# Kernel optimization log

Measured on AMD Instinct MI355X. Metric: run time of the kernel, lower is better.

## Reference

```python
import jax, jax.numpy as jnp
import numpy as np
from jax import lax

DILATIONS = [1, 2, 4, 8, 16, 32, 64, 128, 256, 512] * 2  # 20 layers
C = 128   # residual channels
K = 2     # kernel size


def _causal_dilated_conv(x, w, b, d):
    # x: [B, C, T], w: [2C, C, K], left-pad by d*(K-1) for causality
    pad = d * (K - 1)
    y = lax.conv_general_dilated(
        x, w, window_strides=(1,), padding=[(pad, 0)],
        rhs_dilation=(d,), dimension_numbers=('NCH', 'OIH', 'NCH'))
    return y + b[None, :, None]


def setup_inputs() -> dict:
    key = jax.random.key(0)
    ks = jax.random.split(key, 5)
    L = len(DILATIONS)
    x = jax.random.normal(ks[0], (4, C, 8192), jnp.float32)
    # 0.05 scale keeps activations stable through 20 residual layers
    w_conv = jax.random.normal(ks[1], (L, 2 * C, C, K), jnp.float32) * 0.05
    b_conv = jax.random.normal(ks[2], (L, 2 * C), jnp.float32) * 0.05
    w_out = jax.random.normal(ks[3], (L, C, C), jnp.float32) * 0.05
    b_out = jax.random.normal(ks[4], (L, C), jnp.float32) * 0.05
    return {"x": x, "w_conv": w_conv, "b_conv": b_conv,
            "w_out": w_out, "b_out": b_out}


def reference(x, w_conv, b_conv, w_out, b_out):
    """WaveNet convolution stack: per layer, causal dilated conv -> gated
    tanh*sigmoid -> 1x1 output conv; residual add; collect skips.
    Returns (output [B,C,T], skips [L,B,C,T])."""
    skips = []
    for i, d in enumerate(DILATIONS):
        h = x
        z = _causal_dilated_conv(x, w_conv[i], b_conv[i], d)  # [B, 2C, T]
        g = jnp.tanh(z[:, :C]) * jax.nn.sigmoid(z[:, C:])      # gated, [B, C, T]
        s = jnp.einsum('oc,bct->bot', w_out[i], g) + b_out[i][None, :, None]
        x = s + h  # residual connection
        skips.append(s)
    return x, jnp.stack(skips)
```

## Files before the change

### kernel.cpp

```cpp
#include <hip/hip_runtime.h>
#include <hip/hip_bf16.h>
#include <stdint.h>

using f32x4  = __attribute__((ext_vector_type(4))) float;
using bf16x8 = __attribute__((ext_vector_type(8))) short;
using bf16x4 = __attribute__((ext_vector_type(4))) short;

#define NB   4
#define NC   128
#define NT   8192
#define TL   64
#define NLAYER 20
#define GROWB 272
#define CONVN (NLAYER * 256 * 256)
#define WOUTN (NLAYER * 128 * 128)

__device__ __forceinline__ short f2b(float f) {
  union { float f; unsigned u; } v; v.f = f;
  unsigned r = v.u + 0x7FFFu + ((v.u >> 16) & 1u);
  return (short)(r >> 16);
}

__device__ __forceinline__ float b2f(short s) {
  union { unsigned u; float f; } v;
  v.u = ((unsigned)(unsigned short)s) << 16;
  return v.f;
}

__device__ __forceinline__ f32x4 mfma16(bf16x8 a, bf16x8 b, f32x4 c) {
  return __builtin_amdgcn_mfma_f32_16x16x32_bf16(a, b, c, 0, 0, 0);
}

__device__ __forceinline__ void gl_lds16(const void* g, void* l) {
  __builtin_amdgcn_global_load_lds(
      (const __attribute__((address_space(1))) void*)g,
      (__attribute__((address_space(3))) void*)l, 16, 0, 0);
}

__global__ void transpose_in(const float* __restrict__ x, short* __restrict__ xtb) {
  __shared__ float tile[64][65];
  const int t0 = blockIdx.x * 64;
  const int c0 = blockIdx.y * 64;
  const int b  = blockIdx.z;
  const int lane = threadIdx.x & 63;
  const int r4   = threadIdx.x >> 6;
  #pragma unroll
  for (int i = 0; i < 16; ++i) {
    const int cl = i * 4 + r4;
    tile[cl][lane] = x[((size_t)(b * NC + c0 + cl)) * NT + t0 + lane];
  }
  __syncthreads();
  #pragma unroll
  for (int i = 0; i < 16; ++i) {
    const int tr = i * 4 + r4;
    const float v = tile[lane][tr];
    const int t = t0 + tr, c = c0 + lane;
    const size_t rowB = ((size_t)(b * NT + t)) * 256;
    const int ci = (c >> 3) ^ (t & 7);
    *(short*)((char*)xtb + rowB + ci * 16 + (c & 7) * 2) = f2b(v);
  }
}

__global__ void pack_weights(const float* __restrict__ w_conv,
                             const float* __restrict__ w_out,
                             short* __restrict__ wcb, short* __restrict__ wob) {
  const int idx = blockIdx.x * 256 + threadIdx.x;
  if (idx < CONVN) {
    const int k = idx & 255, o = (idx >> 8) & 255, lyr = idx >> 16;
    const int tap = k >> 7, c = k & 127;
    wcb[idx] = f2b(w_conv[(((size_t)lyr * 256 + o) * 128 + c) * 2 + tap]);
  } else if (idx < CONVN + WOUTN) {
    const int j = idx - CONVN;
    wob[j] = f2b(w_out[j]);
  }
}

__global__ __launch_bounds__(512, 4)
void wavenet_layer(const short* __restrict__ wcb,
                   const float* __restrict__ b_conv,
                   const short* __restrict__ wob,
                   const float* __restrict__ b_out,
                   const short* __restrict__ xbin,
                   short* __restrict__ xbout,
                   float* __restrict__ out,
                   int layer, int dil, int last)
{
  __shared__ char ldsXP[TL * 256];
  __shared__ char ldsXC[TL * 256];
  __shared__ char ldsG[TL * GROWB];

  const int tid = threadIdx.x;
  const int w   = tid >> 6;
  const int l   = tid & 63;
  const int lh  = l & 15;
  const int lq  = l >> 4;
  const int o0  = 16 * w + lq * 4;
  const int uid = (blockIdx.x & 7) * 64 + (blockIdx.x >> 3);
  const int b   = uid >> 7;
  const int t0  = (uid & 127) * 64;

  {
    const char* xcg = (const char*)xbin + ((size_t)(b * NT + t0)) * 256;
    const int off = w * 2048 + l * 16;
    gl_lds16(xcg + off, ldsXC + off);
    gl_lds16(xcg + off + 1024, ldsXC + off + 1024);
  }
  if (t0 >= dil) {
    const char* xpg = (const char*)xbin + ((size_t)(b * NT + t0 - dil)) * 256;
    const int off = w * 2048 + l * 16;
    gl_lds16(xpg + off, ldsXP + off);
    gl_lds16(xpg + off + 1024, ldsXP + off + 1024);
  } else {
    const int row = tid >> 3, j8 = tid & 7;
    const int tp = t0 + row - dil;
    char* dst = ldsXP + row * 256;
    if (tp >= 0) {
      const char* src = (const char*)xbin + ((size_t)(b * NT + tp)) * 256;
      *(bf16x8*)(dst + j8 * 16)       = *(const bf16x8*)(src + j8 * 16);
      *(bf16x8*)(dst + j8 * 16 + 128) = *(const bf16x8*)(src + j8 * 16 + 128);
    } else {
      bf16x8 z = {0, 0, 0, 0, 0, 0, 0, 0};
      *(bf16x8*)(dst + j8 * 16)       = z;
      *(bf16x8*)(dst + j8 * 16 + 128) = z;
    }
  }
  __syncthreads();

  const f32x4 fz = {0.f, 0.f, 0.f, 0.f};
  f32x4 acc1[2][4];
  #pragma unroll
  for (int mi = 0; mi < 2; ++mi)
    #pragma unroll
    for (int n = 0; n < 4; ++n) acc1[mi][n] = fz;

  const short* wl = wcb + (size_t)layer * 65536;
  #pragma unroll
  for (int ks = 0; ks < 8; ++ks) {
    const bf16x8 a0 = *(const bf16x8*)(wl + (16 * w + lh) * 256 + ks * 32 + lq * 8);
    const bf16x8 a1 = *(const bf16x8*)(wl + (128 + 16 * w + lh) * 256 + ks * 32 + lq * 8);
    const char* base = (ks < 4) ? ldsXP : ldsXC;
    const int dd = (ks < 4) ? dil : 0;
    #pragma unroll
    for (int n = 0; n < 4; ++n) {
      const int tt = n * 16 + lh;
      const int ci = ((ks & 3) * 4 + lq) ^ ((tt - dd) & 7);
      const bf16x8 bb = *(const bf16x8*)(base + tt * 256 + ci * 16);
      acc1[0][n] = mfma16(a0, bb, acc1[0][n]);
      acc1[1][n] = mfma16(a1, bb, acc1[1][n]);
    }
  }

  {
    float ba[4], bs[4];
    #pragma unroll
    for (int r = 0; r < 4; ++r) {
      ba[r] = b_conv[layer * 256 + o0 + r];
      bs[r] = b_conv[layer * 256 + 128 + o0 + r];
    }
    #pragma unroll
    for (int n = 0; n < 4; ++n) {
      bf16x4 g4;
      #pragma unroll
      for (int r = 0; r < 4; ++r) {
        const float za = acc1[0][n][r] + ba[r];
        const float zb = acc1[1][n][r] + bs[r];
        const float th = 1.f - 2.f / (1.f + __expf(2.f * za));
        const float sg = 1.f / (1.f + __expf(-zb));
        g4[r] = f2b(th * sg);
      }
      const int tt = n * 16 + lh;
      *(bf16x4*)(ldsG + tt * GROWB + o0 * 2) = g4;
    }
  }
  __syncthreads();

  f32x4 acc2[4];
  #pragma unroll
  for (int n = 0; n < 4; ++n) acc2[n] = fz;
  const short* wol = wob + (size_t)layer * 16384;
  #pragma unroll
  for (int ks = 0; ks < 4; ++ks) {
    const bf16x8 a = *(const bf16x8*)(wol + (16 * w + lh) * 128 + ks * 32 + lq * 8);
    #pragma unroll
    for (int n = 0; n < 4; ++n) {
      const int tt = n * 16 + lh;
      const bf16x8 bb = *(const bf16x8*)(ldsG + tt * GROWB + ks * 64 + lq * 16);
      acc2[n] = mfma16(a, bb, acc2[n]);
    }
  }

  {
    const size_t XOFFS = (size_t)NB * NC * NT;
    float bo[4];
    #pragma unroll
    for (int r = 0; r < 4; ++r) bo[r] = b_out[layer * 128 + o0 + r];
    #pragma unroll
    for (int n = 0; n < 4; ++n) {
      const int tt = n * 16 + lh;
      const int tg = t0 + tt;
      f32x4 s4;
      #pragma unroll
      for (int r = 0; r < 4; ++r) s4[r] = acc2[n][r] + bo[r];
      #pragma unroll
      for (int r = 0; r < 4; ++r)
        out[XOFFS + ((size_t)((layer * NB + b) * NC + o0 + r)) * NT + tg] = s4[r];
      const int ci = (o0 >> 3) ^ (tt & 7);
      const bf16x4 h4 = *(const bf16x4*)(ldsXC + tt * 256 + ci * 16 + (o0 & 7) * 2);
      f32x4 xn;
      #pragma unroll
      for (int r = 0; r < 4; ++r) xn[r] = s4[r] + b2f(h4[r]);
      if (!last) {
        bf16x4 x4;
        #pragma unroll
        for (int r = 0; r < 4; ++r) x4[r] = f2b(xn[r]);
        *(bf16x4*)((char*)xbout + ((size_t)(b * NT + tg)) * 256 + ci * 16 + (o0 & 7) * 2) = x4;
      } else {
        #pragma unroll
        for (int r = 0; r < 4; ++r)
          out[((size_t)(b * NC + o0 + r)) * NT + tg] = xn[r];
      }
    }
  }
}

extern "C" void kernel_launch(void* const* d_in, const int* in_sizes, int n_in,
                              void* d_out, int out_size, void* d_ws, size_t ws_size,
                              hipStream_t stream) {
  const float* x      = (const float*)d_in[0];
  const float* w_conv = (const float*)d_in[1];
  const float* b_conv = (const float*)d_in[2];
  const float* w_out  = (const float*)d_in[3];
  const float* b_out  = (const float*)d_in[4];
  float* out = (float*)d_out;

  const size_t XTN = (size_t)NB * NT * NC;
  short* xb_a = (short*)d_ws;
  short* xb_b = xb_a + XTN;
  short* wcb  = xb_b + XTN;
  short* wob  = wcb + CONVN;

  pack_weights<<<(CONVN + WOUTN + 255) / 256, 256, 0, stream>>>(w_conv, w_out, wcb, wob);
  transpose_in<<<dim3(NT / 64, NC / 64, NB), 256, 0, stream>>>(x, xb_a);

  static const int dil[NLAYER] = {1, 2, 4, 8, 16, 32, 64, 128, 256, 512,
                                  1, 2, 4, 8, 16, 32, 64, 128, 256, 512};
  for (int i = 0; i < NLAYER; ++i) {
    const short* xbi = (i & 1) ? xb_b : xb_a;
    short*       xbo = (i & 1) ? xb_a : xb_b;
    wavenet_layer<<<dim3(512), 512, 0, stream>>>(
        wcb, b_conv, wob, b_out, xbi, xbo, out, i, dil[i],
        (i == NLAYER - 1) ? 1 : 0);
  }
}
```

Before: 381.6 us.

## Fuse first six dilation layers per block with halo recompute in LDS

Adds a kernel that runs layers with dilation 1..32 back-to-back inside one block. It loads a 64-step halo plus the 64-step tile into LDS and recomputes the halo region, so the activation stays in LDS between layers. This replaces 12 of the 20 per-layer launches and cuts their global round trips of the activation, at the cost of about double the MFMA work for the halo, larger LDS use (64KB) and possibly lower occupancy. The input transpose is also vectorised to write 16-byte bf16 chunks instead of single shorts.

```diff
diff --git a/kernel.cpp b/kernel.cpp
--- a/kernel.cpp
+++ b/kernel.cpp
@@ -51,13 +51,16 @@
   }
   __syncthreads();
   #pragma unroll
-  for (int i = 0; i < 16; ++i) {
-    const int tr = i * 4 + r4;
-    const float v = tile[lane][tr];
-    const int t = t0 + tr, c = c0 + lane;
-    const size_t rowB = ((size_t)(b * NT + t)) * 256;
-    const int ci = (c >> 3) ^ (t & 7);
-    *(short*)((char*)xtb + rowB + ci * 16 + (c & 7) * 2) = f2b(v);
+  for (int it = 0; it < 2; ++it) {
+    const int idx = it * 256 + threadIdx.x;
+    const int r  = idx >> 3;
+    const int gi = idx & 7;
+    bf16x8 v;
+    #pragma unroll
+    for (int jj = 0; jj < 8; ++jj) v[jj] = f2b(tile[gi * 8 + jj][r]);
+    const int t = t0 + r;
+    const int ci = ((c0 >> 3) + gi) ^ (t & 7);
+    *(bf16x8*)((char*)xtb + ((size_t)(b * NT + t)) * 256 + ci * 16) = v;
   }
 }
 
@@ -72,6 +75,156 @@
   } else if (idx < CONVN + WOUTN) {
     const int j = idx - CONVN;
     wob[j] = f2b(w_out[j]);
+  }
+}
+
+__global__ __launch_bounds__(512, 4)
+void wavenet_fused6(const short* __restrict__ wcb,
+                    const float* __restrict__ b_conv,
+                    const short* __restrict__ wob,
+                    const float* __restrict__ b_out,
+                    const short* __restrict__ xbin,
+                    short* __restrict__ xbout,
+                    float* __restrict__ out,
+                    int layer0)
+{
+  __shared__ char bufA[128 * 256];
+  __shared__ char bufB[128 * 256];
+  char* ping = bufA;
+  char* pong = bufB;
+
+  const int tid = threadIdx.x;
+  const int w = tid >> 6, l = tid & 63, lh = l & 15, lq = l >> 4;
+  const int o0 = 16 * w + lq * 4;
+  const int uid = (blockIdx.x & 7) * 64 + (blockIdx.x >> 3);
+  const int b   = uid >> 7;
+  const int t0  = (uid & 127) * 64;
+  const bool zhalo = (t0 == 0);
+
+  if (!zhalo) {
+    const char* src = (const char*)xbin + ((size_t)(b * NT + t0 - 64)) * 256;
+    #pragma unroll
+    for (int k = 0; k < 4; ++k)
+      gl_lds16(src + tid * 16 + k * 8192, ping + tid * 16 + k * 8192);
+  } else {
+    bf16x8 z = {0, 0, 0, 0, 0, 0, 0, 0};
+    *(bf16x8*)(ping + tid * 16)        = z;
+    *(bf16x8*)(ping + tid * 16 + 8192) = z;
+    const char* src = (const char*)xbin + ((size_t)(b * NT)) * 256;
+    gl_lds16(src + tid * 16,        ping + 16384 + tid * 16);
+    gl_lds16(src + tid * 16 + 8192, ping + 16384 + tid * 16 + 8192);
+  }
+  __syncthreads();
+
+  const f32x4 fz = {0.f, 0.f, 0.f, 0.f};
+  const size_t XOFFS = (size_t)NB * NC * NT;
+
+  for (int j = 0; j < 6; ++j) {
+    const int layer = layer0 + j;
+    const int d = 1 << j;
+    const short* wl  = wcb + (size_t)layer * 65536;
+    const short* wol = wob + (size_t)layer * 16384;
+    const int u0 = (j < 5) ? 0 : 1;
+
+    for (int u = u0; u < 2; ++u) {
+      f32x4 acc1[2][4];
+      #pragma unroll
+      for (int mi = 0; mi < 2; ++mi)
+        #pragma unroll
+        for (int n = 0; n < 4; ++n) acc1[mi][n] = fz;
+
+      #pragma unroll
+      for (int ks = 0; ks < 8; ++ks) {
+        const bf16x8 a0 = *(const bf16x8*)(wl + (16 * w + lh) * 256 + ks * 32 + lq * 8);
+        const bf16x8 a1 = *(const bf16x8*)(wl + (128 + 16 * w + lh) * 256 + ks * 32 + lq * 8);
+        const int dd = (ks < 4) ? d : 0;
+        #pragma unroll
+        for (int n = 0; n < 4; ++n) {
+          const int wr = u * 64 + n * 16 + lh;
+          int rr = wr - dd; if (rr < 0) rr += 128;
+          const int ci = ((ks & 3) * 4 + lq) ^ (rr & 7);
+          const bf16x8 bb = *(const bf16x8*)(ping + rr * 256 + ci * 16);
+          acc1[0][n] = mfma16(a0, bb, acc1[0][n]);
+          acc1[1][n] = mfma16(a1, bb, acc1[1][n]);
+        }
+      }
+
+      char* G = pong + u * 16384;
+      {
+        float ba[4], bs[4];
+        #pragma unroll
+        for (int r = 0; r < 4; ++r) {
+          ba[r] = b_conv[layer * 256 + o0 + r];
+          bs[r] = b_conv[layer * 256 + 128 + o0 + r];
+        }
+        #pragma unroll
+        for (int n = 0; n < 4; ++n) {
+          bf16x4 g4;
+          #pragma unroll
+          for (int r = 0; r < 4; ++r) {
+            const float za = acc1[0][n][r] + ba[r];
+            const float zb = acc1[1][n][r] + bs[r];
+            const float th = 1.f - 2.f / (1.f + __expf(2.f * za));
+            const float sg = 1.f / (1.f + __expf(-zb));
+            g4[r] = f2b(th * sg);
+          }
+          const int tt = n * 16 + lh;
+          *(bf16x4*)(G + tt * 256 + (((o0 >> 3) ^ (tt & 7)) * 16) + (o0 & 7) * 2) = g4;
+        }
+      }
+      __syncthreads();
+
+      f32x4 acc2[4];
+      #pragma unroll
+      for (int n = 0; n < 4; ++n) acc2[n] = fz;
+      #pragma unroll
+      for (int ks = 0; ks < 4; ++ks) {
+        const bf16x8 a = *(const bf16x8*)(wol + (16 * w + lh) * 128 + ks * 32 + lq * 8);
+        #pragma unroll
+        for (int n = 0; n < 4; ++n) {
+          const int tt = n * 16 + lh;
+          const int ci = (ks * 4 + lq) ^ (tt & 7);
+          const bf16x8 bb = *(const bf16x8*)(G + tt * 256 + ci * 16);
+          acc2[n] = mfma16(a, bb, acc2[n]);
+        }
+      }
+      __syncthreads();
+
+      {
+        float bo[4];
+        #pragma unroll
+        for (int r = 0; r < 4; ++r) bo[r] = b_out[layer * 128 + o0 + r];
+        #pragma unroll
+        for (int n = 0; n < 4; ++n) {
+          const int tt = n * 16 + lh;
+          const int wr = u * 64 + tt;
+          f32x4 s4;
+          #pragma unroll
+          for (int r = 0; r < 4; ++r) s4[r] = acc2[n][r] + bo[r];
+          if (u == 1) {
+            #pragma unroll
+            for (int r = 0; r < 4; ++r)
+              out[XOFFS + ((size_t)((layer * NB + b) * NC + o0 + r)) * NT + (t0 + tt)] = s4[r];
+          }
+          const int ci = (o0 >> 3) ^ (wr & 7);
+          const bf16x4 h4 = *(const bf16x4*)(ping + wr * 256 + ci * 16 + (o0 & 7) * 2);
+          f32x4 xn;
+          #pragma unroll
+          for (int r = 0; r < 4; ++r) xn[r] = s4[r] + b2f(h4[r]);
+          bf16x4 x4;
+          #pragma unroll
+          for (int r = 0; r < 4; ++r) x4[r] = f2b(xn[r]);
+          if (j == 5) {
+            *(bf16x4*)((char*)xbout + ((size_t)(b * NT + t0 + tt)) * 256 + ci * 16 + (o0 & 7) * 2) = x4;
+          } else {
+            if (zhalo && u == 0) { x4[0] = 0; x4[1] = 0; x4[2] = 0; x4[3] = 0; }
+            *(bf16x4*)(pong + wr * 256 + ci * 16 + (o0 & 7) * 2) = x4;
+          }
+        }
+      }
+      if (u == 1 && j < 5) __syncthreads();
+    }
+    { char* t = ping; ping = pong; pong = t; }
   }
 }
 
@@ -234,21 +387,31 @@
   float* out = (float*)d_out;
 
   const size_t XTN = (size_t)NB * NT * NC;
-  short* xb_a = (short*)d_ws;
-  short* xb_b = xb_a + XTN;
-  short* wcb  = xb_b + XTN;
-  short* wob  = wcb + CONVN;
+  short* xb[2];
+  xb[0] = (short*)d_ws;
+  xb[1] = xb[0] + XTN;
+  short* wcb = xb[1] + XTN;
+  short* wob = wcb + CONVN;
 
   pack_weights<<<(CONVN + WOUTN + 255) / 256, 256, 0, stream>>>(w_conv, w_out, wcb, wob);
-  transpose_in<<<dim3(NT / 64, NC / 64, NB), 256, 0, stream>>>(x, xb_a);
-
-  static const int dil[NLAYER] = {1, 2, 4, 8, 16, 32, 64, 128, 256, 512,
-                                  1, 2, 4, 8, 16, 32, 64, 128, 256, 512};
-  for (int i = 0; i < NLAYER; ++i) {
-    const short* xbi = (i & 1) ? xb_b : xb_a;
-    short*       xbo = (i & 1) ? xb_a : xb_b;
+  transpose_in<<<dim3(NT / 64, NC / 64, NB), 256, 0, stream>>>(x, xb[0]);
+
+  int cur = 0;
+  wavenet_fused6<<<dim3(512), 512, 0, stream>>>(wcb, b_conv, wob, b_out,
+                                                xb[cur], xb[cur ^ 1], out, 0);
+  cur ^= 1;
+  for (int i = 6; i <= 9; ++i) {
     wavenet_layer<<<dim3(512), 512, 0, stream>>>(
-        wcb, b_conv, wob, b_out, xbi, xbo, out, i, dil[i],
-        (i == NLAYER - 1) ? 1 : 0);
-  }
-}
+        wcb, b_conv, wob, b_out, xb[cur], xb[cur ^ 1], out, i, 1 << i, 0);
+    cur ^= 1;
+  }
+  wavenet_fused6<<<dim3(512), 512, 0, stream>>>(wcb, b_conv, wob, b_out,
+                                                xb[cur], xb[cur ^ 1], out, 10);
+  cur ^= 1;
+  for (int i = 16; i <= 19; ++i) {
+    wavenet_layer<<<dim3(512), 512, 0, stream>>>(
+        wcb, b_conv, wob, b_out, xb[cur], xb[cur ^ 1], out, i, 1 << (i - 10),
+        (i == 19) ? 1 : 0);
+    cur ^= 1;
+  }
+}
```

New measurement: 666.9 us. +74.8%, slower.

## Stage layer outputs through LDS for coalesced 16-byte global stores

Applied to the files above, without the earlier changes.

Each layer kernel now writes its fp32 skip tile, its bf16 residual tile and the final output into shared memory first. It then stores them to global memory as contiguous 16-byte vectors, replacing scattered 4- and 8-byte per-lane stores. The skip staging buffer reuses the LDS space of the previous-input and gate tiles, so LDS use and occupancy stay the same. The cost is extra barriers and LDS round-trips per block. The final fp32 output is now rounded through bf16, which adds precision error. The input transpose kernel also packs eight channels per thread into one 16-byte store.

```diff
diff --git a/kernel.cpp b/kernel.cpp
--- a/kernel.cpp
+++ b/kernel.cpp
@@ -51,13 +51,16 @@
   }
   __syncthreads();
   #pragma unroll
-  for (int i = 0; i < 16; ++i) {
-    const int tr = i * 4 + r4;
-    const float v = tile[lane][tr];
-    const int t = t0 + tr, c = c0 + lane;
-    const size_t rowB = ((size_t)(b * NT + t)) * 256;
-    const int ci = (c >> 3) ^ (t & 7);
-    *(short*)((char*)xtb + rowB + ci * 16 + (c & 7) * 2) = f2b(v);
+  for (int it = 0; it < 2; ++it) {
+    const int idx = it * 256 + threadIdx.x;
+    const int r  = idx >> 3;
+    const int gi = idx & 7;
+    bf16x8 v;
+    #pragma unroll
+    for (int jj = 0; jj < 8; ++jj) v[jj] = f2b(tile[gi * 8 + jj][r]);
+    const int t = t0 + r;
+    const int ci = ((c0 >> 3) + gi) ^ (t & 7);
+    *(bf16x8*)((char*)xtb + ((size_t)(b * NT + t)) * 256 + ci * 16) = v;
   }
 }
 
@@ -85,9 +88,11 @@
                    float* __restrict__ out,
                    int layer, int dil, int last)
 {
-  __shared__ char ldsXP[TL * 256];
   __shared__ char ldsXC[TL * 256];
-  __shared__ char ldsG[TL * GROWB];
+  __shared__ char ldsSP[TL * 256 + TL * GROWB];
+  char* ldsXP = ldsSP;
+  char* ldsG  = ldsSP + TL * 256;
+  char* ldsS  = ldsSP;
 
   const int tid = threadIdx.x;
   const int w   = tid >> 6;
@@ -188,37 +193,87 @@
       acc2[n] = mfma16(a, bb, acc2[n]);
     }
   }
-
+  __syncthreads();
+
+  f32x4 xn4[4];
   {
-    const size_t XOFFS = (size_t)NB * NC * NT;
     float bo[4];
     #pragma unroll
     for (int r = 0; r < 4; ++r) bo[r] = b_out[layer * 128 + o0 + r];
     #pragma unroll
     for (int n = 0; n < 4; ++n) {
       const int tt = n * 16 + lh;
-      const int tg = t0 + tt;
-      f32x4 s4;
-      #pragma unroll
-      for (int r = 0; r < 4; ++r) s4[r] = acc2[n][r] + bo[r];
-      #pragma unroll
-      for (int r = 0; r < 4; ++r)
-        out[XOFFS + ((size_t)((layer * NB + b) * NC + o0 + r)) * NT + tg] = s4[r];
       const int ci = (o0 >> 3) ^ (tt & 7);
       const bf16x4 h4 = *(const bf16x4*)(ldsXC + tt * 256 + ci * 16 + (o0 & 7) * 2);
-      f32x4 xn;
-      #pragma unroll
-      for (int r = 0; r < 4; ++r) xn[r] = s4[r] + b2f(h4[r]);
+      f32x4 s4, xn;
+      #pragma unroll
+      for (int r = 0; r < 4; ++r) {
+        s4[r] = acc2[n][r] + bo[r];
+        xn[r] = s4[r] + b2f(h4[r]);
+      }
+      #pragma unroll
+      for (int r = 0; r < 4; ++r) {
+        const int o  = o0 + r;
+        const int lg = tt >> 2;
+        const int pg = (lg & 8) | ((lg ^ (o & 7)) & 7);
+        *(float*)(ldsS + o * 256 + pg * 16 + (tt & 3) * 4) = s4[r];
+      }
       if (!last) {
         bf16x4 x4;
         #pragma unroll
         for (int r = 0; r < 4; ++r) x4[r] = f2b(xn[r]);
-        *(bf16x4*)((char*)xbout + ((size_t)(b * NT + tg)) * 256 + ci * 16 + (o0 & 7) * 2) = x4;
+        *(bf16x4*)(ldsXC + tt * 256 + ci * 16 + (o0 & 7) * 2) = x4;
       } else {
+        xn4[n] = xn;
+      }
+    }
+  }
+  __syncthreads();
+
+  const size_t XOFFS = (size_t)NB * NC * NT;
+  {
+    float* skipBase = out + XOFFS + ((size_t)((layer * NB + b) * NC)) * NT + t0;
+    const int j8 = tid & 7;
+    #pragma unroll
+    for (int half = 0; half < 2; ++half) {
+      const int o = half * 64 + (tid >> 3);
+      #pragma unroll
+      for (int k = 0; k < 2; ++k) {
+        const int pg = (k * 8) | ((j8 ^ (o & 7)) & 7);
+        const f32x4 v = *(const f32x4*)(ldsS + o * 256 + pg * 16);
+        *(f32x4*)(skipBase + (size_t)o * NT + j8 * 4 + k * 32) = v;
+      }
+    }
+  }
+  if (!last) {
+    char* dstBase = (char*)xbout + ((size_t)(b * NT + t0)) * 256;
+    #pragma unroll
+    for (int k = 0; k < 2; ++k) {
+      const int idx = k * 512 + tid;
+      const int r = idx >> 4, p = idx & 15;
+      *(f32x4*)(dstBase + r * 256 + p * 16) = *(const f32x4*)(ldsXC + r * 256 + p * 16);
+    }
+  } else {
+    {
+      #pragma unroll
+      for (int n = 0; n < 4; ++n) {
+        const int tt = n * 16 + lh;
         #pragma unroll
         for (int r = 0; r < 4; ++r)
-          out[((size_t)(b * NC + o0 + r)) * NT + tg] = xn[r];
-      }
+          *(short*)(ldsXC + (o0 + r) * 128 + tt * 2) = f2b(xn4[n][r]);
+      }
+    }
+    __syncthreads();
+    float* xBase = out + ((size_t)(b * NC)) * NT + t0;
+    const int j16 = tid & 15;
+    #pragma unroll
+    for (int k = 0; k < 4; ++k) {
+      const int o = k * 32 + (tid >> 4);
+      const bf16x4 v = *(const bf16x4*)(ldsXC + o * 128 + j16 * 8);
+      f32x4 f;
+      #pragma unroll
+      for (int r = 0; r < 4; ++r) f[r] = b2f(v[r]);
+      *(f32x4*)(xBase + (size_t)o * NT + j16 * 4) = f;
     }
   }
 }
@@ -234,21 +289,20 @@
   float* out = (float*)d_out;
 
   const size_t XTN = (size_t)NB * NT * NC;
-  short* xb_a = (short*)d_ws;
-  short* xb_b = xb_a + XTN;
-  short* wcb  = xb_b + XTN;
-  short* wob  = wcb + CONVN;
+  short* xb[2];
+  xb[0] = (short*)d_ws;
+  xb[1] = xb[0] + XTN;
+  short* wcb = xb[1] + XTN;
+  short* wob = wcb + CONVN;
 
   pack_weights<<<(CONVN + WOUTN + 255) / 256, 256, 0, stream>>>(w_conv, w_out, wcb, wob);
-  transpose_in<<<dim3(NT / 64, NC / 64, NB), 256, 0, stream>>>(x, xb_a);
+  transpose_in<<<dim3(NT / 64, NC / 64, NB), 256, 0, stream>>>(x, xb[0]);
 
   static const int dil[NLAYER] = {1, 2, 4, 8, 16, 32, 64, 128, 256, 512,
                                   1, 2, 4, 8, 16, 32, 64, 128, 256, 512};
   for (int i = 0; i < NLAYER; ++i) {
-    const short* xbi = (i & 1) ? xb_b : xb_a;
-    short*       xbo = (i & 1) ? xb_a : xb_b;
     wavenet_layer<<<dim3(512), 512, 0, stream>>>(
-        wcb, b_conv, wob, b_out, xbi, xbo, out, i, dil[i],
+        wcb, b_conv, wob, b_out, xb[i & 1], xb[(i & 1) ^ 1], out, i, dil[i],
         (i == NLAYER - 1) ? 1 : 0);
   }
 }
```

Result: slower. 404.2 us (+5.9%).

## Halve time tile to 32, stage residual in LDS, use nontemporal skip stores

Applied to the files above, without the earlier changes.

Cuts the per-block time tile from 64 to 32 and doubles the grid to 1024 blocks, so more blocks can spread across CUs. The next-layer bf16 activations are written into LDS first and then copied out with one coalesced 16-byte store per thread, replacing scattered 8-byte global stores. Skip outputs are written with nontemporal stores. The G buffer now uses an XOR swizzle instead of padding, and the input transpose writes 16-byte vectors. The cost is that each block's weight fragment loads are now amortized over half as many time steps.

```diff
diff --git a/kernel.cpp b/kernel.cpp
--- a/kernel.cpp
+++ b/kernel.cpp
@@ -9,9 +9,8 @@
 #define NB   4
 #define NC   128
 #define NT   8192
-#define TL   64
+#define TL   32
 #define NLAYER 20
-#define GROWB 272
 #define CONVN (NLAYER * 256 * 256)
 #define WOUTN (NLAYER * 128 * 128)
 
@@ -51,13 +50,16 @@
   }
   __syncthreads();
   #pragma unroll
-  for (int i = 0; i < 16; ++i) {
-    const int tr = i * 4 + r4;
-    const float v = tile[lane][tr];
-    const int t = t0 + tr, c = c0 + lane;
-    const size_t rowB = ((size_t)(b * NT + t)) * 256;
-    const int ci = (c >> 3) ^ (t & 7);
-    *(short*)((char*)xtb + rowB + ci * 16 + (c & 7) * 2) = f2b(v);
+  for (int it = 0; it < 2; ++it) {
+    const int idx = it * 256 + threadIdx.x;
+    const int r  = idx >> 3;
+    const int gi = idx & 7;
+    bf16x8 v;
+    #pragma unroll
+    for (int jj = 0; jj < 8; ++jj) v[jj] = f2b(tile[gi * 8 + jj][r]);
+    const int t = t0 + r;
+    const int ci = ((c0 >> 3) + gi) ^ (t & 7);
+    *(bf16x8*)((char*)xtb + ((size_t)(b * NT + t)) * 256 + ci * 16) = v;
   }
 }
 
@@ -76,18 +78,18 @@
 }
 
 __global__ __launch_bounds__(512, 4)
-void wavenet_layer(const short* __restrict__ wcb,
-                   const float* __restrict__ b_conv,
-                   const short* __restrict__ wob,
-                   const float* __restrict__ b_out,
-                   const short* __restrict__ xbin,
-                   short* __restrict__ xbout,
-                   float* __restrict__ out,
-                   int layer, int dil, int last)
+void wavenet_layer32(const short* __restrict__ wcb,
+                     const float* __restrict__ b_conv,
+                     const short* __restrict__ wob,
+                     const float* __restrict__ b_out,
+                     const short* __restrict__ xbin,
+                     short* __restrict__ xbout,
+                     float* __restrict__ out,
+                     int layer, int dil, int last)
 {
+  __shared__ char ldsXC[TL * 256];
   __shared__ char ldsXP[TL * 256];
-  __shared__ char ldsXC[TL * 256];
-  __shared__ char ldsG[TL * GROWB];
+  __shared__ char ldsG [TL * 256];
 
   const int tid = threadIdx.x;
   const int w   = tid >> 6;
@@ -95,43 +97,37 @@
   const int lh  = l & 15;
   const int lq  = l >> 4;
   const int o0  = 16 * w + lq * 4;
-  const int uid = (blockIdx.x & 7) * 64 + (blockIdx.x >> 3);
-  const int b   = uid >> 7;
-  const int t0  = (uid & 127) * 64;
+  const int uid = (blockIdx.x & 7) * 128 + (blockIdx.x >> 3);
+  const int b   = uid >> 8;
+  const int t0  = (uid & 255) * 32;
 
   {
     const char* xcg = (const char*)xbin + ((size_t)(b * NT + t0)) * 256;
-    const int off = w * 2048 + l * 16;
-    gl_lds16(xcg + off, ldsXC + off);
-    gl_lds16(xcg + off + 1024, ldsXC + off + 1024);
+    gl_lds16(xcg + tid * 16, ldsXC + tid * 16);
   }
   if (t0 >= dil) {
     const char* xpg = (const char*)xbin + ((size_t)(b * NT + t0 - dil)) * 256;
-    const int off = w * 2048 + l * 16;
-    gl_lds16(xpg + off, ldsXP + off);
-    gl_lds16(xpg + off + 1024, ldsXP + off + 1024);
+    gl_lds16(xpg + tid * 16, ldsXP + tid * 16);
   } else {
-    const int row = tid >> 3, j8 = tid & 7;
+    const int row = tid >> 4, p = tid & 15;
     const int tp = t0 + row - dil;
-    char* dst = ldsXP + row * 256;
+    char* dst = ldsXP + row * 256 + p * 16;
     if (tp >= 0) {
       const char* src = (const char*)xbin + ((size_t)(b * NT + tp)) * 256;
-      *(bf16x8*)(dst + j8 * 16)       = *(const bf16x8*)(src + j8 * 16);
-      *(bf16x8*)(dst + j8 * 16 + 128) = *(const bf16x8*)(src + j8 * 16 + 128);
+      *(bf16x8*)dst = *(const bf16x8*)(src + p * 16);
     } else {
       bf16x8 z = {0, 0, 0, 0, 0, 0, 0, 0};
-      *(bf16x8*)(dst + j8 * 16)       = z;
-      *(bf16x8*)(dst + j8 * 16 + 128) = z;
+      *(bf16x8*)dst = z;
     }
   }
   __syncthreads();
 
   const f32x4 fz = {0.f, 0.f, 0.f, 0.f};
-  f32x4 acc1[2][4];
+  f32x4 acc1[2][2];
   #pragma unroll
   for (int mi = 0; mi < 2; ++mi)
     #pragma unroll
-    for (int n = 0; n < 4; ++n) acc1[mi][n] = fz;
+    for (int n = 0; n < 2; ++n) acc1[mi][n] = fz;
 
   const short* wl = wcb + (size_t)layer * 65536;
   #pragma unroll
@@ -141,7 +137,7 @@
     const char* base = (ks < 4) ? ldsXP : ldsXC;
     const int dd = (ks < 4) ? dil : 0;
     #pragma unroll
-    for (int n = 0; n < 4; ++n) {
+    for (int n = 0; n < 2; ++n) {
       const int tt = n * 16 + lh;
       const int ci = ((ks & 3) * 4 + lq) ^ ((tt - dd) & 7);
       const bf16x8 bb = *(const bf16x8*)(base + tt * 256 + ci * 16);
@@ -158,7 +154,7 @@
       bs[r] = b_conv[layer * 256 + 128 + o0 + r];
     }
     #pragma unroll
-    for (int n = 0; n < 4; ++n) {
+    for (int n = 0; n < 2; ++n) {
       bf16x4 g4;
       #pragma unroll
       for (int r = 0; r < 4; ++r) {
@@ -169,57 +165,64 @@
         g4[r] = f2b(th * sg);
       }
       const int tt = n * 16 + lh;
-      *(bf16x4*)(ldsG + tt * GROWB + o0 * 2) = g4;
+      const int ci = (o0 >> 3) ^ (tt & 7);
+      *(bf16x4*)(ldsG + tt * 256 + ci * 16 + (o0 & 7) * 2) = g4;
     }
   }
   __syncthreads();
 
-  f32x4 acc2[4];
-  #pragma unroll
-  for (int n = 0; n < 4; ++n) acc2[n] = fz;
+  f32x4 acc2[2];
+  #pragma unroll
+  for (int n = 0; n < 2; ++n) acc2[n] = fz;
   const short* wol = wob + (size_t)layer * 16384;
   #pragma unroll
   for (int ks = 0; ks < 4; ++ks) {
     const bf16x8 a = *(const bf16x8*)(wol + (16 * w + lh) * 128 + ks * 32 + lq * 8);
     #pragma unroll
-    for (int n = 0; n < 4; ++n) {
-      const int tt = n * 16 + lh;
-      const bf16x8 bb = *(const bf16x8*)(ldsG + tt * GROWB + ks * 64 + lq * 16);
+    for (int n = 0; n < 2; ++n) {
+      const int tt = n * 16 + lh;
+      const int ci = (ks * 4 + lq) ^ (tt & 7);
+      const bf16x8 bb = *(const bf16x8*)(ldsG + tt * 256 + ci * 16);
       acc2[n] = mfma16(a, bb, acc2[n]);
     }
   }
 
+  const size_t XOFFS = (size_t)NB * NC * NT;
   {
-    const size_t XOFFS = (size_t)NB * NC * NT;
     float bo[4];
     #pragma unroll
     for (int r = 0; r < 4; ++r) bo[r] = b_out[layer * 128 + o0 + r];
-    #pragma unroll
-    for (int n = 0; n < 4; ++n) {
-      const int tt = n * 16 + lh;
-      const int tg = t0 + tt;
-      f32x4 s4;
-      #pragma unroll
-      for (int r = 0; r < 4; ++r) s4[r] = acc2[n][r] + bo[r];
-      #pragma unroll
-      for (int r = 0; r < 4; ++r)
-        out[XOFFS + ((size_t)((layer * NB + b) * NC + o0 + r)) * NT + tg] = s4[r];
+    float* skipBase = out + XOFFS + ((size_t)((layer * NB + b) * NC)) * NT + t0;
+    float* xBase    = out + ((size_t)(b * NC)) * NT + t0;
+    #pragma unroll
+    for (int n = 0; n < 2; ++n) {
+      const int tt = n * 16 + lh;
       const int ci = (o0 >> 3) ^ (tt & 7);
       const bf16x4 h4 = *(const bf16x4*)(ldsXC + tt * 256 + ci * 16 + (o0 & 7) * 2);
-      f32x4 xn;
+      f32x4 s4, xn;
       #pragma unroll
-      for (int r = 0; r < 4; ++r) xn[r] = s4[r] + b2f(h4[r]);
+      for (int r = 0; r < 4; ++r) {
+        s4[r] = acc2[n][r] + bo[r];
+        xn[r] = s4[r] + b2f(h4[r]);
+        __builtin_nontemporal_store(s4[r], skipBase + (size_t)(o0 + r) * NT + tt);
+      }
       if (!last) {
         bf16x4 x4;
         #pragma unroll
         for (int r = 0; r < 4; ++r) x4[r] = f2b(xn[r]);
-        *(bf16x4*)((char*)xbout + ((size_t)(b * NT + tg)) * 256 + ci * 16 + (o0 & 7) * 2) = x4;
+        *(bf16x4*)(ldsXC + tt * 256 + ci * 16 + (o0 & 7) * 2) = x4;
       } else {
         #pragma unroll
         for (int r = 0; r < 4; ++r)
-          out[((size_t)(b * NC + o0 + r)) * NT + tg] = xn[r];
+          __builtin_nontemporal_store(xn[r], xBase + (size_t)(o0 + r) * NT + tt);
       }
     }
+  }
+
+  if (!last) {
+    __syncthreads();
+    char* dstBase = (char*)xbout + ((size_t)(b * NT + t0)) * 256;
+    *(f32x4*)(dstBase + tid * 16) = *(const f32x4*)(ldsXC + tid * 16);
   }
 }
 
@@ -234,21 +237,20 @@
   float* out = (float*)d_out;
 
   const size_t XTN = (size_t)NB * NT * NC;
-  short* xb_a = (short*)d_ws;
-  short* xb_b = xb_a + XTN;
-  short* wcb  = xb_b + XTN;
-  short* wob  = wcb + CONVN;
+  short* xb[2];
+  xb[0] = (short*)d_ws;
+  xb[1] = xb[0] + XTN;
+  short* wcb = xb[1] + XTN;
+  short* wob = wcb + CONVN;
 
   pack_weights<<<(CONVN + WOUTN + 255) / 256, 256, 0, stream>>>(w_conv, w_out, wcb, wob);
-  transpose_in<<<dim3(NT / 64, NC / 64, NB), 256, 0, stream>>>(x, xb_a);
+  transpose_in<<<dim3(NT / 64, NC / 64, NB), 256, 0, stream>>>(x, xb[0]);
 
   static const int dil[NLAYER] = {1, 2, 4, 8, 16, 32, 64, 128, 256, 512,
                                   1, 2, 4, 8, 16, 32, 64, 128, 256, 512};
   for (int i = 0; i < NLAYER; ++i) {
-    const short* xbi = (i & 1) ? xb_b : xb_a;
-    short*       xbo = (i & 1) ? xb_a : xb_b;
-    wavenet_layer<<<dim3(512), 512, 0, stream>>>(
-        wcb, b_conv, wob, b_out, xbi, xbo, out, i, dil[i],
+    wavenet_layer32<<<dim3(1024), 512, 0, stream>>>(
+        wcb, b_conv, wob, b_out, xb[i & 1], xb[(i & 1) ^ 1], out, i, dil[i],
         (i == NLAYER - 1) ? 1 : 0);
   }
 }
```

Measured after the change: 480.1 us. 25.8% more time.
